# Kernel optimization log

Measured on AMD Instinct MI355X. Metric: run time of the kernel, lower is better.

Reference implementation:

```python
import jax, jax.numpy as jnp
import numpy as np

CTX = 2048
D_IN = 1024
D_OUT = 1024
BATCH = 8


def setup_inputs() -> dict:
    key = jax.random.key(0)
    k1, k2, k3, k4 = jax.random.split(key, 4)
    x = jax.random.normal(k1, (BATCH, CTX, D_IN), dtype=jnp.float32)
    # nn.Linear weight is [out, in]; store pre-transposed as [in, out] for x @ W
    Wk = jax.random.normal(k2, (D_IN, D_OUT), dtype=jnp.float32) * (1.0 / np.sqrt(D_IN))
    Wq = jax.random.normal(k3, (D_IN, D_OUT), dtype=jnp.float32) * (1.0 / np.sqrt(D_IN))
    Wv = jax.random.normal(k4, (D_IN, D_OUT), dtype=jnp.float32) * (1.0 / np.sqrt(D_IN))
    return {"x": x, "Wq": Wq, "Wk": Wk, "Wv": Wv}


def reference(x, Wq, Wk, Wv):
    # projections: [b, s, d_out]
    q = jnp.einsum('bsi,io->bso', x, Wq)
    k = jnp.einsum('bsi,io->bso', x, Wk)
    v = jnp.einsum('bsi,io->bso', x, Wv)
    s = q.shape[1]
    scale = 1.0 / jnp.sqrt(jnp.asarray(q.shape[-1], q.dtype))
    att = jnp.einsum('bqd,bkd->bqk', q, k) * scale  # [b, s, s]
    # additive causal mask: 0 on/below diagonal, -inf above
    causal = jnp.tril(jnp.ones((s, s), dtype=bool))
    att = jnp.where(causal, att, -jnp.inf)
    att = jax.nn.softmax(att, axis=-1)
    return jnp.einsum('bqk,bkd->bqd', att, v)
```

## Files before the change

### kernel.cpp

```cpp
#include <hip/hip_runtime.h>
#include <stdint.h>

typedef unsigned short u16;
typedef short bf16x8 __attribute__((ext_vector_type(8)));
typedef float f32x4 __attribute__((ext_vector_type(4)));

#define CTX 2048
#define DIN 1024
#define DOUT 1024
#define NB 8

__device__ __forceinline__ u16 f2bf(float f) {
  uint32_t u = __builtin_bit_cast(uint32_t, f);
  u += 0x7FFFu + ((u >> 16) & 1u);
  return (u16)(u >> 16);
}

__device__ __forceinline__ void gld_lds16(const u16* g, const u16* lds) {
  __builtin_amdgcn_global_load_lds(
      (const __attribute__((address_space(1))) uint32_t*)(unsigned long long)(const void*)g,
      (__attribute__((address_space(3))) uint32_t*)(uint32_t)(unsigned long long)(const void*)lds,
      16, 0, 0);
}

#define SBAR() asm volatile("s_barrier" ::: "memory")
#define VMCNT3() asm volatile("s_waitcnt vmcnt(3)" ::: "memory")
#define VMCNT0() asm volatile("s_waitcnt vmcnt(0)" ::: "memory")
#define SCHED0() __builtin_amdgcn_sched_barrier(0)

template <typename EPI>
__device__ __forceinline__ void gemm128x256(const u16* __restrict__ A, int lda,
                                            const u16* __restrict__ Bt, int ldb,
                                            int m0, int n0, int K, EPI&& epi) {
  __shared__ __align__(16) u16 lds[36864];

  const int t = threadIdx.x;
  const int lane = t & 63;
  const int w = t >> 6;
  const int wm = w >> 2;
  const int wn = w & 3;
  const int l15 = lane & 15;
  const int l16 = lane >> 4;
  const int nkt = K >> 5;

  f32x4 acc[4][4];
#pragma unroll
  for (int i = 0; i < 4; ++i)
#pragma unroll
    for (int j = 0; j < 4; ++j) acc[i][j] = {0.f, 0.f, 0.f, 0.f};

  const u16* gA = A + (size_t)(m0 + w * 16 + l15) * lda + l16 * 8;
  const u16* gB = Bt + (size_t)(n0 + w * 16 + l15) * ldb + l16 * 8;
  const size_t ldJB = (size_t)128 * ldb;

  auto STAGE = [&](int kbuf, int T) {
    const size_t koff = (size_t)T * 32;
    u16* base = lds + kbuf * 12288;
    gld_lds16(gA + koff, base + w * 512);
    gld_lds16(gB + koff, base + 4096 + w * 512);
    gld_lds16(gB + koff + ldJB, base + 8192 + w * 512);
  };

  STAGE(0, 0);
  STAGE(1, 1);
  VMCNT3();
  SBAR();

  int cb = 0;
  int sb = 2;
  for (int T = 0; T < nkt; ++T) {
    if (T + 2 < nkt) STAGE(sb, T + 2);

    const u16* bufA = lds + cb * 12288 + (wm * 4) * 512 + lane * 8;
    const u16* bufB = lds + cb * 12288 + 4096 + (wn * 4) * 512 + lane * 8;
    bf16x8 ar[4], br[4];
#pragma unroll
    for (int fr = 0; fr < 4; ++fr)
      ar[fr] = *reinterpret_cast<const bf16x8*>(bufA + fr * 512);
#pragma unroll
    for (int nc = 0; nc < 4; ++nc)
      br[nc] = *reinterpret_cast<const bf16x8*>(bufB + nc * 512);

    __builtin_amdgcn_s_setprio(1);
#pragma unroll
    for (int fr = 0; fr < 4; ++fr)
#pragma unroll
      for (int nc = 0; nc < 4; ++nc)
        acc[fr][nc] = __builtin_amdgcn_mfma_f32_16x16x32_bf16(ar[fr], br[nc],
                                                              acc[fr][nc], 0, 0, 0);
    __builtin_amdgcn_s_setprio(0);
    SCHED0();
    if (T + 2 < nkt) {
      VMCNT3();
    } else {
      VMCNT0();
    }
    SBAR();
    cb = (cb == 2) ? 0 : cb + 1;
    sb = (sb == 2) ? 0 : sb + 1;
  }

  epi(acc, wm * 64 + l16 * 4, wn * 64 + l15);
}

__global__ __launch_bounds__(256) void k_cvt_x(const float* __restrict__ x,
                                               u16* __restrict__ xb) {
  const int idx = (blockIdx.x * 256 + threadIdx.x) * 4;
  const float4 v = *reinterpret_cast<const float4*>(x + idx);
  ushort4 o;
  o.x = f2bf(v.x); o.y = f2bf(v.y); o.z = f2bf(v.z); o.w = f2bf(v.w);
  *reinterpret_cast<ushort4*>(xb + idx) = o;
}

__global__ __launch_bounds__(256) void k_cvt_wt(const float* __restrict__ W,
                                                u16* __restrict__ Wt) {
  __shared__ u16 tile[64][65];
  const int bc = blockIdx.x;
  const int tr0 = (bc >> 4) * 64;
  const int tc0 = (bc & 15) * 64;
  const int t = threadIdx.x;
  const int col = t & 63, rr = t >> 6;
#pragma unroll
  for (int p = 0; p < 16; ++p) {
    const int row = rr * 16 + p;
    tile[row][col] = f2bf(W[(size_t)(tr0 + row) * DOUT + tc0 + col]);
  }
  __syncthreads();
#pragma unroll
  for (int p = 0; p < 16; ++p) {
    const int row = rr * 16 + p;
    Wt[(size_t)(tc0 + row) * DIN + tr0 + col] = tile[col][row];
  }
}

__global__ __launch_bounds__(512, 4) void k_proj(const u16* __restrict__ xb,
                                                 const u16* __restrict__ Wt,
                                                 u16* __restrict__ qkb,
                                                 u16* __restrict__ vT) {
  const int wg = (blockIdx.x & 7) * 192 + (blockIdx.x >> 3);
  const int m0 = (wg / 12) * 128, n0 = (wg % 12) * 256;
  gemm128x256(xb, DIN, Wt, DIN, m0, n0, DIN,
              [&](const f32x4(&acc)[4][4], int r0, int c0) {
                if (n0 < 2 * DOUT) {
#pragma unroll
                  for (int fr = 0; fr < 4; ++fr)
#pragma unroll
                    for (int nc = 0; nc < 4; ++nc) {
                      const int r = m0 + r0 + fr * 16;
                      const int c = n0 + c0 + nc * 16;
#pragma unroll
                      for (int i = 0; i < 4; ++i)
                        qkb[(size_t)(r + i) * 2048 + c] = f2bf(acc[fr][nc][i]);
                    }
                } else {
                  const int b = m0 >> 11;
                  const int sl = (m0 & (CTX - 1)) + r0;
                  u16* C = vT + (size_t)b * DOUT * CTX;
#pragma unroll
                  for (int fr = 0; fr < 4; ++fr)
#pragma unroll
                    for (int nc = 0; nc < 4; ++nc) {
                      const int d = n0 - 2 * DOUT + c0 + nc * 16;
                      const int s = sl + fr * 16;
                      ushort4 o;
                      o.x = f2bf(acc[fr][nc][0]);
                      o.y = f2bf(acc[fr][nc][1]);
                      o.z = f2bf(acc[fr][nc][2]);
                      o.w = f2bf(acc[fr][nc][3]);
                      *reinterpret_cast<ushort4*>(C + (size_t)d * CTX + s) = o;
                    }
                }
              });
}

__global__ __launch_bounds__(512, 4) void k_score(const u16* __restrict__ qkb,
                                                  float* __restrict__ S) {
  const int u = (blockIdx.x & 7) * 72 + (blockIdx.x >> 3);
  const int b = u / 72, v = u % 72;
  int it = 0, pre = 0;
  while (pre + (it / 2 + 1) <= v) { pre += it / 2 + 1; ++it; }
  const int jt = v - pre;
  const u16* Aq = qkb + (size_t)b * CTX * 2048;
  float* C = S + ((size_t)b << 22);
  const int m0 = it * 128, n0 = jt * 256;
  gemm128x256(Aq, 2048, Aq + 1024, 2048, m0, n0, DOUT,
              [&](const f32x4(&acc)[4][4], int r0, int c0) {
#pragma unroll
                for (int fr = 0; fr < 4; ++fr)
#pragma unroll
                  for (int nc = 0; nc < 4; ++nc) {
                    const int r = m0 + r0 + fr * 16;
                    const int c = n0 + c0 + nc * 16;
#pragma unroll
                    for (int i = 0; i < 4; ++i)
                      C[(size_t)(r + i) * CTX + c] = acc[fr][nc][i] * 0.03125f;
                  }
              });
}

__global__ __launch_bounds__(256) void k_softmax(float* __restrict__ Sws) {
  const int row = blockIdx.x;
  const int b = row >> 11, i = row & (CTX - 1);
  const float* srow = Sws + ((size_t)b << 22) + ((size_t)i << 11);
  u16* prow = (u16*)(Sws + ((size_t)b << 22)) + ((size_t)i << 12);
  const int t = threadIdx.x;
  const int j0 = t * 8;
  float vv[8];
  if (j0 <= i) {
    const float4 v0 = *reinterpret_cast<const float4*>(srow + j0);
    const float4 v1 = *reinterpret_cast<const float4*>(srow + j0 + 4);
    vv[0] = v0.x; vv[1] = v0.y; vv[2] = v0.z; vv[3] = v0.w;
    vv[4] = v1.x; vv[5] = v1.y; vv[6] = v1.z; vv[7] = v1.w;
  } else {
#pragma unroll
    for (int p = 0; p < 8; ++p) vv[p] = -3.0e38f;
  }
  float mx = -3.0e38f;
#pragma unroll
  for (int p = 0; p < 8; ++p) {
    vv[p] = (j0 + p <= i) ? vv[p] : -3.0e38f;
    mx = fmaxf(mx, vv[p]);
  }
#pragma unroll
  for (int off = 32; off > 0; off >>= 1) mx = fmaxf(mx, __shfl_xor(mx, off));
  __shared__ float redm[4], reds[4];
  const int lane = t & 63, wid = t >> 6;
  if (lane == 0) redm[wid] = mx;
  __syncthreads();
  mx = fmaxf(fmaxf(redm[0], redm[1]), fmaxf(redm[2], redm[3]));
  float e[8], s = 0.f;
#pragma unroll
  for (int p = 0; p < 8; ++p) {
    e[p] = __expf(vv[p] - mx);
    s += e[p];
  }
#pragma unroll
  for (int off = 32; off > 0; off >>= 1) s += __shfl_xor(s, off);
  if (lane == 0) reds[wid] = s;
  __syncthreads();
  s = reds[0] + reds[1] + reds[2] + reds[3];
  const float inv = 1.0f / s;
  ushort4 o0, o1;
  o0.x = (j0 + 0 <= i) ? f2bf(e[0] * inv) : (u16)0;
  o0.y = (j0 + 1 <= i) ? f2bf(e[1] * inv) : (u16)0;
  o0.z = (j0 + 2 <= i) ? f2bf(e[2] * inv) : (u16)0;
  o0.w = (j0 + 3 <= i) ? f2bf(e[3] * inv) : (u16)0;
  o1.x = (j0 + 4 <= i) ? f2bf(e[4] * inv) : (u16)0;
  o1.y = (j0 + 5 <= i) ? f2bf(e[5] * inv) : (u16)0;
  o1.z = (j0 + 6 <= i) ? f2bf(e[6] * inv) : (u16)0;
  o1.w = (j0 + 7 <= i) ? f2bf(e[7] * inv) : (u16)0;
  *reinterpret_cast<ushort4*>(prow + j0) = o0;
  *reinterpret_cast<ushort4*>(prow + j0 + 4) = o1;
}

__global__ __launch_bounds__(512, 4) void k_out(const float* __restrict__ Sws,
                                                const u16* __restrict__ vT,
                                                float* __restrict__ out) {
  const int idx = blockIdx.x;
  const int it = 15 - (idx >> 5);
  const int b = (idx >> 2) & 7;
  const int nt = idx & 3;
  const u16* P = (const u16*)(Sws + ((size_t)b << 22));
  const u16* Bt = vT + (size_t)b * DOUT * CTX;
  float* C = out + (size_t)b * CTX * DOUT;
  const int m0 = it * 128, n0 = nt * 256;
  gemm128x256(P, 2 * CTX, Bt, CTX, m0, n0, (it + 1) * 128,
              [&](const f32x4(&acc)[4][4], int r0, int c0) {
#pragma unroll
                for (int fr = 0; fr < 4; ++fr)
#pragma unroll
                  for (int nc = 0; nc < 4; ++nc) {
                    const int r = m0 + r0 + fr * 16;
                    const int c = n0 + c0 + nc * 16;
#pragma unroll
                    for (int i = 0; i < 4; ++i)
                      C[(size_t)(r + i) * DOUT + c] = acc[fr][nc][i];
                  }
              });
}

extern "C" void kernel_launch(void* const* d_in, const int* in_sizes, int n_in,
                              void* d_out, int out_size, void* d_ws, size_t ws_size,
                              hipStream_t stream) {
  (void)in_sizes; (void)n_in; (void)out_size; (void)ws_size;
  const float* x = (const float*)d_in[0];
  const float* Wq = (const float*)d_in[1];
  const float* Wk = (const float*)d_in[2];
  const float* Wv = (const float*)d_in[3];
  float* out = (float*)d_out;
  uint8_t* ws = (uint8_t*)d_ws;

  float* S = (float*)ws;
  u16* xb = (u16*)ws;
  u16* Wt_all = (u16*)(ws + 33554432ull);
  u16* qkb = (u16*)(ws + 134217728ull);
  u16* vT = (u16*)(ws + 201326592ull);

  k_cvt_x<<<16384, 256, 0, stream>>>(x, xb);
  k_cvt_wt<<<256, 256, 0, stream>>>(Wq, Wt_all);
  k_cvt_wt<<<256, 256, 0, stream>>>(Wk, Wt_all + 1024ull * 1024);
  k_cvt_wt<<<256, 256, 0, stream>>>(Wv, Wt_all + 2048ull * 1024);
  k_proj<<<1536, 512, 0, stream>>>(xb, Wt_all, qkb, vT);
  k_score<<<576, 512, 0, stream>>>(qkb, S);
  k_softmax<<<NB * CTX, 256, 0, stream>>>(S);
  k_out<<<512, 512, 0, stream>>>(S, vT, out);
}
```

Before: 351.9 us.

## Fuse conversion kernels, use 256x256 projection tiles, pair causal output tiles

Merges the x and three weight conversion kernels into a single launch, which removes launch overhead. The projection GEMM moves to 1024-thread blocks with 256x256 tiles, so each staged B tile is reused across more rows. The output GEMM gives each block one long and one short causal row tile to balance the triangular work, and halves the grid. The larger projection blocks use more LDS and registers per block, so fewer blocks may fit on each CU.

Result: faster. 309.2 us (-12.1%).

```diff
diff --git a/kernel.cpp b/kernel.cpp
--- a/kernel.cpp
+++ b/kernel.cpp
@@ -25,14 +25,14 @@
 
 #define SBAR() asm volatile("s_barrier" ::: "memory")
 #define VMCNT3() asm volatile("s_waitcnt vmcnt(3)" ::: "memory")
+#define VMCNT2() asm volatile("s_waitcnt vmcnt(2)" ::: "memory")
 #define VMCNT0() asm volatile("s_waitcnt vmcnt(0)" ::: "memory")
-#define SCHED0() __builtin_amdgcn_sched_barrier(0)
 
 template <typename EPI>
-__device__ __forceinline__ void gemm128x256(const u16* __restrict__ A, int lda,
-                                            const u16* __restrict__ Bt, int ldb,
-                                            int m0, int n0, int K, EPI&& epi) {
-  __shared__ __align__(16) u16 lds[36864];
+__device__ __forceinline__ void gemm256w16(const u16* __restrict__ A, int lda,
+                                           const u16* __restrict__ Bt, int ldb,
+                                           int m0, int n0, int K, EPI&& epi) {
+  __shared__ __align__(16) u16 lds[49152];
 
   const int t = threadIdx.x;
   const int lane = t & 63;
@@ -51,6 +51,79 @@
 
   const u16* gA = A + (size_t)(m0 + w * 16 + l15) * lda + l16 * 8;
   const u16* gB = Bt + (size_t)(n0 + w * 16 + l15) * ldb + l16 * 8;
+
+  auto STAGE = [&](int kbuf, int T) {
+    const size_t koff = (size_t)T * 32;
+    u16* base = lds + kbuf * 16384;
+    gld_lds16(gA + koff, base + w * 512);
+    gld_lds16(gB + koff, base + 8192 + w * 512);
+  };
+
+  STAGE(0, 0);
+  STAGE(1, 1);
+  VMCNT2();
+  SBAR();
+
+  int cb = 0;
+  int sb = 2;
+  for (int T = 0; T < nkt; ++T) {
+    if (T + 2 < nkt) STAGE(sb, T + 2);
+
+    const u16* bufA = lds + cb * 16384 + (wm * 4) * 512 + lane * 8;
+    const u16* bufB = lds + cb * 16384 + 8192 + (wn * 4) * 512 + lane * 8;
+    bf16x8 ar[4], br[4];
+#pragma unroll
+    for (int fr = 0; fr < 4; ++fr)
+      ar[fr] = *reinterpret_cast<const bf16x8*>(bufA + fr * 512);
+#pragma unroll
+    for (int nc = 0; nc < 4; ++nc)
+      br[nc] = *reinterpret_cast<const bf16x8*>(bufB + nc * 512);
+
+    __builtin_amdgcn_s_setprio(1);
+#pragma unroll
+    for (int fr = 0; fr < 4; ++fr)
+#pragma unroll
+      for (int nc = 0; nc < 4; ++nc)
+        acc[fr][nc] = __builtin_amdgcn_mfma_f32_16x16x32_bf16(ar[fr], br[nc],
+                                                              acc[fr][nc], 0, 0, 0);
+    __builtin_amdgcn_s_setprio(0);
+    __builtin_amdgcn_sched_barrier(0);
+    if (T + 2 < nkt) {
+      VMCNT2();
+    } else {
+      VMCNT0();
+    }
+    SBAR();
+    cb = (cb == 2) ? 0 : cb + 1;
+    sb = (sb == 2) ? 0 : sb + 1;
+  }
+
+  epi(acc, wm * 64 + l16 * 4, wn * 64 + l15);
+}
+
+template <typename EPI>
+__device__ __forceinline__ void gemm128x256(const u16* __restrict__ A, int lda,
+                                            const u16* __restrict__ Bt, int ldb,
+                                            int m0, int n0, int K, EPI&& epi) {
+  __shared__ __align__(16) u16 lds[36864];
+
+  const int t = threadIdx.x;
+  const int lane = t & 63;
+  const int w = t >> 6;
+  const int wm = w >> 2;
+  const int wn = w & 3;
+  const int l15 = lane & 15;
+  const int l16 = lane >> 4;
+  const int nkt = K >> 5;
+
+  f32x4 acc[4][4];
+#pragma unroll
+  for (int i = 0; i < 4; ++i)
+#pragma unroll
+    for (int j = 0; j < 4; ++j) acc[i][j] = {0.f, 0.f, 0.f, 0.f};
+
+  const u16* gA = A + (size_t)(m0 + w * 16 + l15) * lda + l16 * 8;
+  const u16* gB = Bt + (size_t)(n0 + w * 16 + l15) * ldb + l16 * 8;
   const size_t ldJB = (size_t)128 * ldb;
 
   auto STAGE = [&](int kbuf, int T) {
@@ -89,7 +162,7 @@
         acc[fr][nc] = __builtin_amdgcn_mfma_f32_16x16x32_bf16(ar[fr], br[nc],
                                                               acc[fr][nc], 0, 0, 0);
     __builtin_amdgcn_s_setprio(0);
-    SCHED0();
+    __builtin_amdgcn_sched_barrier(0);
     if (T + 2 < nkt) {
       VMCNT3();
     } else {
@@ -103,74 +176,80 @@
   epi(acc, wm * 64 + l16 * 4, wn * 64 + l15);
 }
 
-__global__ __launch_bounds__(256) void k_cvt_x(const float* __restrict__ x,
-                                               u16* __restrict__ xb) {
-  const int idx = (blockIdx.x * 256 + threadIdx.x) * 4;
-  const float4 v = *reinterpret_cast<const float4*>(x + idx);
-  ushort4 o;
-  o.x = f2bf(v.x); o.y = f2bf(v.y); o.z = f2bf(v.z); o.w = f2bf(v.w);
-  *reinterpret_cast<ushort4*>(xb + idx) = o;
-}
-
-__global__ __launch_bounds__(256) void k_cvt_wt(const float* __restrict__ W,
-                                                u16* __restrict__ Wt) {
+__global__ __launch_bounds__(256) void k_cvt_all(const float* __restrict__ x,
+                                                 const float* __restrict__ Wq,
+                                                 const float* __restrict__ Wk,
+                                                 const float* __restrict__ Wv,
+                                                 u16* __restrict__ xb,
+                                                 u16* __restrict__ Wt_all) {
   __shared__ u16 tile[64][65];
-  const int bc = blockIdx.x;
-  const int tr0 = (bc >> 4) * 64;
-  const int tc0 = (bc & 15) * 64;
   const int t = threadIdx.x;
-  const int col = t & 63, rr = t >> 6;
-#pragma unroll
-  for (int p = 0; p < 16; ++p) {
-    const int row = rr * 16 + p;
-    tile[row][col] = f2bf(W[(size_t)(tr0 + row) * DOUT + tc0 + col]);
-  }
-  __syncthreads();
-#pragma unroll
-  for (int p = 0; p < 16; ++p) {
-    const int row = rr * 16 + p;
-    Wt[(size_t)(tc0 + row) * DIN + tr0 + col] = tile[col][row];
-  }
-}
-
-__global__ __launch_bounds__(512, 4) void k_proj(const u16* __restrict__ xb,
-                                                 const u16* __restrict__ Wt,
-                                                 u16* __restrict__ qkb,
-                                                 u16* __restrict__ vT) {
-  const int wg = (blockIdx.x & 7) * 192 + (blockIdx.x >> 3);
-  const int m0 = (wg / 12) * 128, n0 = (wg % 12) * 256;
-  gemm128x256(xb, DIN, Wt, DIN, m0, n0, DIN,
-              [&](const f32x4(&acc)[4][4], int r0, int c0) {
-                if (n0 < 2 * DOUT) {
-#pragma unroll
-                  for (int fr = 0; fr < 4; ++fr)
-#pragma unroll
-                    for (int nc = 0; nc < 4; ++nc) {
-                      const int r = m0 + r0 + fr * 16;
-                      const int c = n0 + c0 + nc * 16;
-#pragma unroll
-                      for (int i = 0; i < 4; ++i)
-                        qkb[(size_t)(r + i) * 2048 + c] = f2bf(acc[fr][nc][i]);
-                    }
-                } else {
-                  const int b = m0 >> 11;
-                  const int sl = (m0 & (CTX - 1)) + r0;
-                  u16* C = vT + (size_t)b * DOUT * CTX;
-#pragma unroll
-                  for (int fr = 0; fr < 4; ++fr)
-#pragma unroll
-                    for (int nc = 0; nc < 4; ++nc) {
-                      const int d = n0 - 2 * DOUT + c0 + nc * 16;
-                      const int s = sl + fr * 16;
-                      ushort4 o;
-                      o.x = f2bf(acc[fr][nc][0]);
-                      o.y = f2bf(acc[fr][nc][1]);
-                      o.z = f2bf(acc[fr][nc][2]);
-                      o.w = f2bf(acc[fr][nc][3]);
-                      *reinterpret_cast<ushort4*>(C + (size_t)d * CTX + s) = o;
-                    }
-                }
-              });
+  if (blockIdx.x < 768) {
+    const int sel = blockIdx.x >> 8;
+    const int bc = blockIdx.x & 255;
+    const float* W = (sel == 0) ? Wq : ((sel == 1) ? Wk : Wv);
+    u16* Wt = Wt_all + ((size_t)sel << 20);
+    const int tr0 = (bc >> 4) * 64;
+    const int tc0 = (bc & 15) * 64;
+    const int col = t & 63, rr = t >> 6;
+#pragma unroll
+    for (int p = 0; p < 16; ++p) {
+      const int row = rr * 16 + p;
+      tile[row][col] = f2bf(W[(size_t)(tr0 + row) * DOUT + tc0 + col]);
+    }
+    __syncthreads();
+#pragma unroll
+    for (int p = 0; p < 16; ++p) {
+      const int row = rr * 16 + p;
+      Wt[(size_t)(tc0 + row) * DIN + tr0 + col] = tile[col][row];
+    }
+  } else {
+    const int idx = ((blockIdx.x - 768) * 256 + t) * 4;
+    const float4 v = *reinterpret_cast<const float4*>(x + idx);
+    ushort4 o;
+    o.x = f2bf(v.x); o.y = f2bf(v.y); o.z = f2bf(v.z); o.w = f2bf(v.w);
+    *reinterpret_cast<ushort4*>(xb + idx) = o;
+  }
+}
+
+__global__ __launch_bounds__(1024, 4) void k_proj(const u16* __restrict__ xb,
+                                                  const u16* __restrict__ Wt,
+                                                  u16* __restrict__ qkb,
+                                                  u16* __restrict__ vT) {
+  const int wg = (blockIdx.x & 7) * 96 + (blockIdx.x >> 3);
+  const int m0 = (wg / 12) * 256, n0 = (wg % 12) * 256;
+  gemm256w16(xb, DIN, Wt, DIN, m0, n0, DIN,
+             [&](const f32x4(&acc)[4][4], int r0, int c0) {
+               if (n0 < 2 * DOUT) {
+#pragma unroll
+                 for (int fr = 0; fr < 4; ++fr)
+#pragma unroll
+                   for (int nc = 0; nc < 4; ++nc) {
+                     const int r = m0 + r0 + fr * 16;
+                     const int c = n0 + c0 + nc * 16;
+#pragma unroll
+                     for (int i = 0; i < 4; ++i)
+                       qkb[(size_t)(r + i) * 2048 + c] = f2bf(acc[fr][nc][i]);
+                   }
+               } else {
+                 const int b = m0 >> 11;
+                 const int sl = (m0 & (CTX - 1)) + r0;
+                 u16* C = vT + (size_t)b * DOUT * CTX;
+#pragma unroll
+                 for (int fr = 0; fr < 4; ++fr)
+#pragma unroll
+                   for (int nc = 0; nc < 4; ++nc) {
+                     const int d = n0 - 2 * DOUT + c0 + nc * 16;
+                     const int s = sl + fr * 16;
+                     ushort4 o;
+                     o.x = f2bf(acc[fr][nc][0]);
+                     o.y = f2bf(acc[fr][nc][1]);
+                     o.z = f2bf(acc[fr][nc][2]);
+                     o.w = f2bf(acc[fr][nc][3]);
+                     *reinterpret_cast<ushort4*>(C + (size_t)d * CTX + s) = o;
+                   }
+               }
+             });
 }
 
 __global__ __launch_bounds__(512, 4) void k_score(const u16* __restrict__ qkb,
@@ -257,26 +336,32 @@
                                                 const u16* __restrict__ vT,
                                                 float* __restrict__ out) {
   const int idx = blockIdx.x;
-  const int it = 15 - (idx >> 5);
+  const int pp = idx >> 5;
   const int b = (idx >> 2) & 7;
   const int nt = idx & 3;
   const u16* P = (const u16*)(Sws + ((size_t)b << 22));
   const u16* Bt = vT + (size_t)b * DOUT * CTX;
   float* C = out + (size_t)b * CTX * DOUT;
-  const int m0 = it * 128, n0 = nt * 256;
-  gemm128x256(P, 2 * CTX, Bt, CTX, m0, n0, (it + 1) * 128,
-              [&](const f32x4(&acc)[4][4], int r0, int c0) {
-#pragma unroll
-                for (int fr = 0; fr < 4; ++fr)
-#pragma unroll
-                  for (int nc = 0; nc < 4; ++nc) {
-                    const int r = m0 + r0 + fr * 16;
-                    const int c = n0 + c0 + nc * 16;
-#pragma unroll
-                    for (int i = 0; i < 4; ++i)
-                      C[(size_t)(r + i) * DOUT + c] = acc[fr][nc][i];
-                  }
-              });
+#pragma unroll 1
+  for (int s = 0; s < 2; ++s) {
+    const int it = s ? pp : (15 - pp);
+    const int m0 = it * 128, n0 = nt * 256;
+    gemm128x256(P, 2 * CTX, Bt, CTX, m0, n0, (it + 1) * 128,
+                [&](const f32x4(&acc)[4][4], int r0, int c0) {
+#pragma unroll
+                  for (int fr = 0; fr < 4; ++fr)
+#pragma unroll
+                    for (int nc = 0; nc < 4; ++nc) {
+                      const int r = m0 + r0 + fr * 16;
+                      const int c = n0 + c0 + nc * 16;
+#pragma unroll
+                      for (int i = 0; i < 4; ++i)
+                        C[(size_t)(r + i) * DOUT + c] = acc[fr][nc][i];
+                    }
+                });
+    VMCNT0();
+    SBAR();
+  }
 }
 
 extern "C" void kernel_launch(void* const* d_in, const int* in_sizes, int n_in,
@@ -296,12 +381,9 @@
   u16* qkb = (u16*)(ws + 134217728ull);
   u16* vT = (u16*)(ws + 201326592ull);
 
-  k_cvt_x<<<16384, 256, 0, stream>>>(x, xb);
-  k_cvt_wt<<<256, 256, 0, stream>>>(Wq, Wt_all);
-  k_cvt_wt<<<256, 256, 0, stream>>>(Wk, Wt_all + 1024ull * 1024);
-  k_cvt_wt<<<256, 256, 0, stream>>>(Wv, Wt_all + 2048ull * 1024);
-  k_proj<<<1536, 512, 0, stream>>>(xb, Wt_all, qkb, vT);
+  k_cvt_all<<<768 + 16384, 256, 0, stream>>>(x, Wq, Wk, Wv, xb, Wt_all);
+  k_proj<<<768, 1024, 0, stream>>>(xb, Wt_all, qkb, vT);
   k_score<<<576, 512, 0, stream>>>(qkb, S);
   k_softmax<<<NB * CTX, 256, 0, stream>>>(S);
-  k_out<<<512, 512, 0, stream>>>(S, vT, out);
-}
+  k_out<<<256, 512, 0, stream>>>(S, vT, out);
+}
```
